# Kernel tuning notes

Hardware: AMD Instinct MI355X
Metric: run time of the kernel (lower is better)

Reference implementation:

```python
import jax, jax.numpy as jnp
import numpy as np

N_NODES = 100000
N_EDGES = 1600000
IN_C = 128
HID = 128
LAT = 64
N_LAYERS = 3
N_GRAPHS = 1000


def setup_inputs() -> dict:
    key = jax.random.key(0)
    ks = jax.random.split(key, 16)
    x = jax.random.normal(ks[0], (N_NODES, IN_C), dtype=jnp.float32)
    edge_index = jax.random.randint(ks[1], (2, N_EDGES), 0, N_NODES, dtype=jnp.int64)
    batch = jnp.sort(jax.random.randint(ks[2], (N_NODES,), 0, N_GRAPHS, dtype=jnp.int64))
    s = 1.0 / np.sqrt(HID)
    # per-layer GIN MLP params (in_c == hidden for all layers since IN_C == HID)
    W1 = jax.random.normal(ks[3], (N_LAYERS, IN_C, HID), dtype=jnp.float32) * s
    b1 = jnp.zeros((N_LAYERS, HID), dtype=jnp.float32)
    W2 = jax.random.normal(ks[4], (N_LAYERS, HID, HID), dtype=jnp.float32) * s
    b2 = jnp.zeros((N_LAYERS, HID), dtype=jnp.float32)
    W_mu = jax.random.normal(ks[5], (HID, LAT), dtype=jnp.float32) * s
    b_mu = jnp.zeros((LAT,), dtype=jnp.float32)
    W_lv = jax.random.normal(ks[6], (HID, LAT), dtype=jnp.float32) * s
    b_lv = jnp.zeros((LAT,), dtype=jnp.float32)
    return {"x": x, "edge_index": edge_index, "batch": batch,
            "W1": W1, "b1": b1, "W2": W2, "b2": b2,
            "W_mu": W_mu, "b_mu": b_mu, "W_lv": W_lv, "b_lv": b_lv}


def reference(x, edge_index, batch, W1, b1, W2, b2, W_mu, b_mu, W_lv, b_lv):
    src, dst = edge_index[0], edge_index[1]
    h = x
    for i in range(N_LAYERS):
        # GINConv (eps=0): h' = MLP(h + sum_{j in N(i)} h_j); scatter-add over edges
        agg = h + jax.ops.segment_sum(h[src], dst, num_segments=N_NODES)
        h = jax.nn.relu(agg @ W1[i] + b1[i])
        h = jax.nn.relu(h @ W2[i] + b2[i])
        h = jax.nn.relu(h)  # extra ReLU in forward after conv (idempotent here)
    # global_add_pool: segment-sum nodes into graphs
    g = jax.ops.segment_sum(h, batch, num_segments=N_GRAPHS)  # [G, HID]
    mu = g @ W_mu + b_mu
    logvar = g @ W_lv + b_lv
    return (mu, logvar)
```

## Files before the change

### kernel.cpp

```cpp
#include <hip/hip_runtime.h>

#define N_NODES 100000
#define N_EDGES 1600000
#define HID 128
#define LAT 64
#define N_LAYERS 3
#define N_GRAPHS 1000
#define CAP 64
#define NBIN 391
#define MAXBIN 4608
#define ACHUNK 8192
#define ABLOCKS ((N_EDGES + ACHUNK - 1) / ACHUNK)
#define CVT_BLOCKS (N_NODES * HID / 4 / 256)

typedef short bf16x8 __attribute__((ext_vector_type(8)));
typedef float f32x4 __attribute__((ext_vector_type(4)));

__device__ __forceinline__ float bf2f(unsigned short h) {
    union { unsigned int u; float f; } c;
    c.u = ((unsigned int)h) << 16;
    return c.f;
}
__device__ __forceinline__ unsigned short f2bf(float f) {
    union { float f; unsigned int u; } c;
    c.f = f;
    unsigned int u = c.u;
    return (unsigned short)((u + 0x7fffu + ((u >> 16) & 1u)) >> 16);
}
__device__ __forceinline__ unsigned int pack2(float a, float b) {
    return (unsigned int)f2bf(a) | ((unsigned int)f2bf(b) << 16);
}
__device__ __forceinline__ void addrow(float* acc, uint4 w) {
    acc[0] += bf2f((unsigned short)w.x); acc[1] += bf2f((unsigned short)(w.x >> 16));
    acc[2] += bf2f((unsigned short)w.y); acc[3] += bf2f((unsigned short)(w.y >> 16));
    acc[4] += bf2f((unsigned short)w.z); acc[5] += bf2f((unsigned short)(w.z >> 16));
    acc[6] += bf2f((unsigned short)w.w); acc[7] += bf2f((unsigned short)(w.w >> 16));
}

__global__ __launch_bounds__(256) void prep_kernel(const float* __restrict__ x,
                                                   unsigned short* __restrict__ xb,
                                                   const float* __restrict__ W1,
                                                   const float* __restrict__ W2,
                                                   unsigned short* __restrict__ Wt) {
    int blk = blockIdx.x;
    if (blk < 6) {
        const float* W = ((blk & 1) ? W2 : W1) + (size_t)(blk >> 1) * HID * HID;
        unsigned short* D = Wt + (size_t)blk * HID * HID;
        for (int idx = threadIdx.x; idx < HID * HID; idx += 256) {
            int n = idx >> 7, k = idx & 127;
            D[n * HID + k] = f2bf(W[k * HID + n]);
        }
        return;
    }
    int i = (blk - 6) * 256 + threadIdx.x;
    if (i >= N_NODES * HID / 4) return;
    float4 v = ((const float4*)x)[i];
    ((uint2*)xb)[i] = make_uint2(pack2(v.x, v.y), pack2(v.z, v.w));
}

__global__ __launch_bounds__(256) void binA_kernel(const int* __restrict__ ei,
                                                   int* __restrict__ gcnt,
                                                   unsigned int* __restrict__ ebin) {
    __shared__ unsigned int scount[NBIN];
    __shared__ unsigned int sfill[NBIN];
    int t = threadIdx.x;
    int base = blockIdx.x * ACHUNK;
    int n = N_EDGES - base;
    if (n > ACHUNK) n = ACHUNK;
    for (int i = t; i < NBIN; i += 256) scount[i] = 0u;
    __syncthreads();
    for (int i = t; i < n; i += 256) {
        int d = ei[N_EDGES + base + i];
        atomicAdd(&scount[d >> 8], 1u);
    }
    __syncthreads();
    for (int b = t; b < NBIN; b += 256) {
        unsigned int c = scount[b];
        sfill[b] = c ? (unsigned int)atomicAdd(&gcnt[b], (int)c) : 0u;
    }
    __syncthreads();
    for (int i = t; i < n; i += 256) {
        int s = ei[base + i];
        int d = ei[N_EDGES + base + i];
        int b = d >> 8;
        unsigned int pos = atomicAdd(&sfill[b], 1u);
        ebin[(size_t)b * MAXBIN + pos] = ((unsigned int)(d & 255) << 24) | (unsigned int)s;
    }
}

__global__ __launch_bounds__(256) void binB_kernel(const unsigned int* __restrict__ ebin,
                                                   const int* __restrict__ gcnt,
                                                   int* __restrict__ cnt,
                                                   int* __restrict__ csr) {
    __shared__ int scnt[256];
    int b = blockIdx.x;
    int t = threadIdx.x;
    scnt[t] = 0;
    __syncthreads();
    int n0 = b << 8;
    int c = gcnt[b];
    const unsigned int* src = ebin + (size_t)b * MAXBIN;
    for (int i = t; i < c; i += 256) {
        unsigned int e = src[i];
        int dl = (int)(e >> 24);
        int slot = atomicAdd(&scnt[dl], 1);
        csr[(size_t)(n0 + dl) * CAP + slot] = (int)(e & 0xFFFFFFu);
    }
    __syncthreads();
    int node = n0 + t;
    if (node < N_NODES) cnt[node] = scnt[t];
}

__global__ __launch_bounds__(256) void gather_kernel(const unsigned short* __restrict__ h,
                                                     const int* __restrict__ cnt,
                                                     const int* __restrict__ csr,
                                                     unsigned short* __restrict__ agg) {
    int t = threadIdx.x;
    int node = blockIdx.x * 16 + (t >> 4);
    int q = t & 15;
    if (node >= N_NODES) return;
    const int* nl = csr + (size_t)node * CAP;
    int deg = cnt[node];
    float acc[8] = {0.f, 0.f, 0.f, 0.f, 0.f, 0.f, 0.f, 0.f};
    addrow(acc, *(const uint4*)(h + (size_t)node * HID + q * 8));
    int e = 0;
    for (; e + 8 <= deg; e += 8) {
        int s0 = nl[e], s1 = nl[e + 1], s2 = nl[e + 2], s3 = nl[e + 3];
        int s4 = nl[e + 4], s5 = nl[e + 5], s6 = nl[e + 6], s7 = nl[e + 7];
        uint4 w0 = *(const uint4*)(h + (size_t)s0 * HID + q * 8);
        uint4 w1 = *(const uint4*)(h + (size_t)s1 * HID + q * 8);
        uint4 w2 = *(const uint4*)(h + (size_t)s2 * HID + q * 8);
        uint4 w3 = *(const uint4*)(h + (size_t)s3 * HID + q * 8);
        uint4 w4 = *(const uint4*)(h + (size_t)s4 * HID + q * 8);
        uint4 w5 = *(const uint4*)(h + (size_t)s5 * HID + q * 8);
        uint4 w6 = *(const uint4*)(h + (size_t)s6 * HID + q * 8);
        uint4 w7 = *(const uint4*)(h + (size_t)s7 * HID + q * 8);
        addrow(acc, w0); addrow(acc, w1); addrow(acc, w2); addrow(acc, w3);
        addrow(acc, w4); addrow(acc, w5); addrow(acc, w6); addrow(acc, w7);
    }
    for (; e + 4 <= deg; e += 4) {
        int s0 = nl[e], s1 = nl[e + 1], s2 = nl[e + 2], s3 = nl[e + 3];
        uint4 w0 = *(const uint4*)(h + (size_t)s0 * HID + q * 8);
        uint4 w1 = *(const uint4*)(h + (size_t)s1 * HID + q * 8);
        uint4 w2 = *(const uint4*)(h + (size_t)s2 * HID + q * 8);
        uint4 w3 = *(const uint4*)(h + (size_t)s3 * HID + q * 8);
        addrow(acc, w0); addrow(acc, w1); addrow(acc, w2); addrow(acc, w3);
    }
    for (; e < deg; ++e) {
        addrow(acc, *(const uint4*)(h + (size_t)nl[e] * HID + q * 8));
    }
    uint4 o;
    o.x = pack2(acc[0], acc[1]);
    o.y = pack2(acc[2], acc[3]);
    o.z = pack2(acc[4], acc[5]);
    o.w = pack2(acc[6], acc[7]);
    *(uint4*)(agg + (size_t)node * HID + q * 8) = o;
}

__global__ __launch_bounds__(256) void mlp_kernel(const unsigned short* __restrict__ A,
                                                  const unsigned short* __restrict__ W1t,
                                                  const float* __restrict__ b1,
                                                  const unsigned short* __restrict__ W2t,
                                                  const float* __restrict__ b2,
                                                  unsigned short* __restrict__ out,
                                                  const int* __restrict__ batch,
                                                  float* __restrict__ gpool) {
    __shared__ unsigned short sA[64][136];
    __shared__ unsigned short sW[128][40];
    __shared__ float sb[128];
    __shared__ int sbatch[64];
    const int t = threadIdx.x;
    const int w = t >> 6;
    const int l = t & 63;
    const int lm = l & 15;
    const int quad = l >> 4;
    const int row0 = blockIdx.x * 64;

    for (int idx = t; idx < 1024; idx += 256) {
        int r = idx >> 4, c = idx & 15;
        int grow = row0 + r;
        uint4 v = make_uint4(0u, 0u, 0u, 0u);
        if (grow < N_NODES) v = *(const uint4*)(A + (size_t)grow * HID + c * 8);
        *(uint4*)&sA[r][c * 8] = v;
    }
    if (gpool && t < 64) {
        int n = row0 + t;
        sbatch[t] = (n < N_NODES) ? batch[n] : -1;
    }

    const unsigned short* Wt[2] = {W1t, W2t};
    const float* bias[2] = {b1, b2};

    for (int p = 0; p < 2; ++p) {
        if (t < 128) sb[t] = bias[p][t];
        f32x4 acc[8];
#pragma unroll
        for (int nt = 0; nt < 8; ++nt) acc[nt] = (f32x4){0.f, 0.f, 0.f, 0.f};

        for (int kc = 0; kc < 4; ++kc) {
            __syncthreads();
            for (int idx = t; idx < 512; idx += 256) {
                int n = idx >> 2, kq = idx & 3;
                *(uint4*)&sW[n][kq * 8] =
                    *(const uint4*)(Wt[p] + (size_t)n * HID + kc * 32 + kq * 8);
            }
            __syncthreads();
            bf16x8 a = *(const bf16x8*)&sA[w * 16 + lm][kc * 32 + quad * 8];
#pragma unroll
            for (int nt = 0; nt < 8; ++nt) {
                bf16x8 b = *(const bf16x8*)&sW[nt * 16 + lm][quad * 8];
                acc[nt] = __builtin_amdgcn_mfma_f32_16x16x32_bf16(a, b, acc[nt], 0, 0, 0);
            }
        }
        __syncthreads();
#pragma unroll
        for (int nt = 0; nt < 8; ++nt) {
            float bv = sb[nt * 16 + lm];
#pragma unroll
            for (int r = 0; r < 4; ++r) {
                int m = w * 16 + quad * 4 + r;
                float val = fmaxf(acc[nt][r] + bv, 0.f);
                sA[m][nt * 16 + lm] = f2bf(val);
            }
        }
        __syncthreads();
    }

    if (!gpool) {
        for (int idx = t; idx < 1024; idx += 256) {
            int r = idx >> 4, c = idx & 15;
            int grow = row0 + r;
            if (grow < N_NODES)
                *(uint4*)(out + (size_t)grow * HID + c * 8) = *(const uint4*)&sA[r][c * 8];
        }
    } else {
        int c = t & 127;
        int r0 = (t >> 7) * 32;
        float acc = 0.f;
        int cur = sbatch[r0];
        for (int r = r0; r < r0 + 32; ++r) {
            int b = sbatch[r];
            if (b < 0) break;
            if (b != cur) {
                atomicAdd(&gpool[(size_t)cur * HID + c], acc);
                acc = 0.f;
                cur = b;
            }
            acc += bf2f(sA[r][c]);
        }
        if (cur >= 0) atomicAdd(&gpool[(size_t)cur * HID + c], acc);
    }
}

__global__ __launch_bounds__(128) void head_kernel(const float* __restrict__ g,
                                                   const float* __restrict__ Wmu,
                                                   const float* __restrict__ bmu,
                                                   const float* __restrict__ Wlv,
                                                   const float* __restrict__ blv,
                                                   float* __restrict__ out) {
    __shared__ float sg[HID];
    int gi = blockIdx.x;
    sg[threadIdx.x] = g[(size_t)gi * HID + threadIdx.x];
    __syncthreads();
    int j = threadIdx.x & 63;
    bool is_lv = threadIdx.x >= 64;
    const float* W = is_lv ? Wlv : Wmu;
    float acc = is_lv ? blv[j] : bmu[j];
    for (int k = 0; k < HID; ++k) acc = fmaf(sg[k], W[k * LAT + j], acc);
    out[(is_lv ? (size_t)N_GRAPHS * LAT : 0) + (size_t)gi * LAT + j] = acc;
}

extern "C" void kernel_launch(void* const* d_in, const int* in_sizes, int n_in,
                              void* d_out, int out_size, void* d_ws, size_t ws_size,
                              hipStream_t stream) {
    const float* x     = (const float*)d_in[0];
    const int*   ei    = (const int*)d_in[1];
    const int*   batch = (const int*)d_in[2];
    const float* W1    = (const float*)d_in[3];
    const float* b1    = (const float*)d_in[4];
    const float* W2    = (const float*)d_in[5];
    const float* b2    = (const float*)d_in[6];
    const float* Wmu   = (const float*)d_in[7];
    const float* bmu   = (const float*)d_in[8];
    const float* Wlv   = (const float*)d_in[9];
    const float* blv   = (const float*)d_in[10];
    float* out = (float*)d_out;

    unsigned short* xb   = (unsigned short*)d_ws;
    unsigned short* agg  = xb + (size_t)N_NODES * HID;
    unsigned short* hbuf = agg + (size_t)N_NODES * HID;
    int* csr = (int*)(hbuf + (size_t)N_NODES * HID);
    unsigned int* ebin = (unsigned int*)(csr + (size_t)N_NODES * CAP);
    unsigned short* Wt = (unsigned short*)(ebin + (size_t)NBIN * MAXBIN);
    float* g  = (float*)(Wt + (size_t)6 * HID * HID);
    int* gcnt = (int*)(g + (size_t)N_GRAPHS * HID);
    int* cnt  = gcnt + NBIN + 1;

    hipMemsetAsync(g, 0, (size_t)N_GRAPHS * HID * sizeof(float) + (NBIN + 1) * sizeof(int),
                   stream);

    binA_kernel<<<ABLOCKS, 256, 0, stream>>>(ei, gcnt, ebin);
    binB_kernel<<<NBIN, 256, 0, stream>>>(ebin, gcnt, cnt, csr);

    prep_kernel<<<CVT_BLOCKS + 6, 256, 0, stream>>>(x, xb, W1, W2, Wt);

    const unsigned short* hcur = xb;
    for (int i = 0; i < N_LAYERS; ++i) {
        bool last = (i == N_LAYERS - 1);
        gather_kernel<<<(N_NODES + 15) / 16, 256, 0, stream>>>(hcur, cnt, csr, agg);
        mlp_kernel<<<(N_NODES + 63) / 64, 256, 0, stream>>>(
            agg, Wt + (size_t)(2 * i) * HID * HID, b1 + (size_t)i * HID,
            Wt + (size_t)(2 * i + 1) * HID * HID, b2 + (size_t)i * HID, hbuf,
            batch, last ? g : nullptr);
        hcur = hbuf;
    }
    head_kernel<<<N_GRAPHS, 128, 0, stream>>>(g, Wmu, bmu, Wlv, blv, out);
}
```

Baseline: 419.3 us.

## Fuse neighbor gather into MLP kernel and ping-pong hidden buffers

Merges the per-layer gather and MLP kernels into one. Each 64-row block aggregates its nodes' neighbor rows straight into shared memory before the two matmuls. This removes the round trip of the agg buffer through global memory and one launch per layer. Two alternating h buffers replace the single one, since a fused layer cannot overwrite the h it is still reading. The cost is lower gather parallelism per block (4 sequential row groups per thread) and gather latency that is no longer overlapped across separate kernel waves.

```diff
diff --git a/kernel.cpp b/kernel.cpp
--- a/kernel.cpp
+++ b/kernel.cpp
@@ -111,60 +111,16 @@
     if (node < N_NODES) cnt[node] = scnt[t];
 }
 
-__global__ __launch_bounds__(256) void gather_kernel(const unsigned short* __restrict__ h,
-                                                     const int* __restrict__ cnt,
-                                                     const int* __restrict__ csr,
-                                                     unsigned short* __restrict__ agg) {
-    int t = threadIdx.x;
-    int node = blockIdx.x * 16 + (t >> 4);
-    int q = t & 15;
-    if (node >= N_NODES) return;
-    const int* nl = csr + (size_t)node * CAP;
-    int deg = cnt[node];
-    float acc[8] = {0.f, 0.f, 0.f, 0.f, 0.f, 0.f, 0.f, 0.f};
-    addrow(acc, *(const uint4*)(h + (size_t)node * HID + q * 8));
-    int e = 0;
-    for (; e + 8 <= deg; e += 8) {
-        int s0 = nl[e], s1 = nl[e + 1], s2 = nl[e + 2], s3 = nl[e + 3];
-        int s4 = nl[e + 4], s5 = nl[e + 5], s6 = nl[e + 6], s7 = nl[e + 7];
-        uint4 w0 = *(const uint4*)(h + (size_t)s0 * HID + q * 8);
-        uint4 w1 = *(const uint4*)(h + (size_t)s1 * HID + q * 8);
-        uint4 w2 = *(const uint4*)(h + (size_t)s2 * HID + q * 8);
-        uint4 w3 = *(const uint4*)(h + (size_t)s3 * HID + q * 8);
-        uint4 w4 = *(const uint4*)(h + (size_t)s4 * HID + q * 8);
-        uint4 w5 = *(const uint4*)(h + (size_t)s5 * HID + q * 8);
-        uint4 w6 = *(const uint4*)(h + (size_t)s6 * HID + q * 8);
-        uint4 w7 = *(const uint4*)(h + (size_t)s7 * HID + q * 8);
-        addrow(acc, w0); addrow(acc, w1); addrow(acc, w2); addrow(acc, w3);
-        addrow(acc, w4); addrow(acc, w5); addrow(acc, w6); addrow(acc, w7);
-    }
-    for (; e + 4 <= deg; e += 4) {
-        int s0 = nl[e], s1 = nl[e + 1], s2 = nl[e + 2], s3 = nl[e + 3];
-        uint4 w0 = *(const uint4*)(h + (size_t)s0 * HID + q * 8);
-        uint4 w1 = *(const uint4*)(h + (size_t)s1 * HID + q * 8);
-        uint4 w2 = *(const uint4*)(h + (size_t)s2 * HID + q * 8);
-        uint4 w3 = *(const uint4*)(h + (size_t)s3 * HID + q * 8);
-        addrow(acc, w0); addrow(acc, w1); addrow(acc, w2); addrow(acc, w3);
-    }
-    for (; e < deg; ++e) {
-        addrow(acc, *(const uint4*)(h + (size_t)nl[e] * HID + q * 8));
-    }
-    uint4 o;
-    o.x = pack2(acc[0], acc[1]);
-    o.y = pack2(acc[2], acc[3]);
-    o.z = pack2(acc[4], acc[5]);
-    o.w = pack2(acc[6], acc[7]);
-    *(uint4*)(agg + (size_t)node * HID + q * 8) = o;
-}
-
-__global__ __launch_bounds__(256) void mlp_kernel(const unsigned short* __restrict__ A,
-                                                  const unsigned short* __restrict__ W1t,
-                                                  const float* __restrict__ b1,
-                                                  const unsigned short* __restrict__ W2t,
-                                                  const float* __restrict__ b2,
-                                                  unsigned short* __restrict__ out,
-                                                  const int* __restrict__ batch,
-                                                  float* __restrict__ gpool) {
+__global__ __launch_bounds__(256) void fused_kernel(const unsigned short* __restrict__ h,
+                                                    const int* __restrict__ cnt,
+                                                    const int* __restrict__ csr,
+                                                    const unsigned short* __restrict__ W1t,
+                                                    const float* __restrict__ b1,
+                                                    const unsigned short* __restrict__ W2t,
+                                                    const float* __restrict__ b2,
+                                                    unsigned short* __restrict__ out,
+                                                    const int* __restrict__ batch,
+                                                    float* __restrict__ gpool) {
     __shared__ unsigned short sA[64][136];
     __shared__ unsigned short sW[128][40];
     __shared__ float sb[128];
@@ -176,16 +132,56 @@
     const int quad = l >> 4;
     const int row0 = blockIdx.x * 64;
 
-    for (int idx = t; idx < 1024; idx += 256) {
-        int r = idx >> 4, c = idx & 15;
-        int grow = row0 + r;
-        uint4 v = make_uint4(0u, 0u, 0u, 0u);
-        if (grow < N_NODES) v = *(const uint4*)(A + (size_t)grow * HID + c * 8);
-        *(uint4*)&sA[r][c * 8] = v;
-    }
     if (gpool && t < 64) {
         int n = row0 + t;
         sbatch[t] = (n < N_NODES) ? batch[n] : -1;
+    }
+
+    {
+        const int q = t & 15;
+        const int g16 = t >> 4;
+        for (int r4 = 0; r4 < 4; ++r4) {
+            int rloc = (r4 << 4) + g16;
+            int node = row0 + rloc;
+            float acc[8] = {0.f, 0.f, 0.f, 0.f, 0.f, 0.f, 0.f, 0.f};
+            if (node < N_NODES) {
+                addrow(acc, *(const uint4*)(h + (size_t)node * HID + q * 8));
+                const int* nl = csr + (size_t)node * CAP;
+                int deg = cnt[node];
+                int e = 0;
+                for (; e + 8 <= deg; e += 8) {
+                    int s0 = nl[e], s1 = nl[e + 1], s2 = nl[e + 2], s3 = nl[e + 3];
+                    int s4 = nl[e + 4], s5 = nl[e + 5], s6 = nl[e + 6], s7 = nl[e + 7];
+                    uint4 w0 = *(const uint4*)(h + (size_t)s0 * HID + q * 8);
+                    uint4 w1 = *(const uint4*)(h + (size_t)s1 * HID + q * 8);
+                    uint4 w2 = *(const uint4*)(h + (size_t)s2 * HID + q * 8);
+                    uint4 w3 = *(const uint4*)(h + (size_t)s3 * HID + q * 8);
+                    uint4 w4 = *(const uint4*)(h + (size_t)s4 * HID + q * 8);
+                    uint4 w5 = *(const uint4*)(h + (size_t)s5 * HID + q * 8);
+                    uint4 w6 = *(const uint4*)(h + (size_t)s6 * HID + q * 8);
+                    uint4 w7 = *(const uint4*)(h + (size_t)s7 * HID + q * 8);
+                    addrow(acc, w0); addrow(acc, w1); addrow(acc, w2); addrow(acc, w3);
+                    addrow(acc, w4); addrow(acc, w5); addrow(acc, w6); addrow(acc, w7);
+                }
+                for (; e + 4 <= deg; e += 4) {
+                    int s0 = nl[e], s1 = nl[e + 1], s2 = nl[e + 2], s3 = nl[e + 3];
+                    uint4 w0 = *(const uint4*)(h + (size_t)s0 * HID + q * 8);
+                    uint4 w1 = *(const uint4*)(h + (size_t)s1 * HID + q * 8);
+                    uint4 w2 = *(const uint4*)(h + (size_t)s2 * HID + q * 8);
+                    uint4 w3 = *(const uint4*)(h + (size_t)s3 * HID + q * 8);
+                    addrow(acc, w0); addrow(acc, w1); addrow(acc, w2); addrow(acc, w3);
+                }
+                for (; e < deg; ++e) {
+                    addrow(acc, *(const uint4*)(h + (size_t)nl[e] * HID + q * 8));
+                }
+            }
+            uint4 o;
+            o.x = pack2(acc[0], acc[1]);
+            o.y = pack2(acc[2], acc[3]);
+            o.z = pack2(acc[4], acc[5]);
+            o.w = pack2(acc[6], acc[7]);
+            *(uint4*)&sA[rloc][q * 8] = o;
+        }
     }
 
     const unsigned short* Wt[2] = {W1t, W2t};
@@ -287,9 +283,9 @@
     float* out = (float*)d_out;
 
     unsigned short* xb   = (unsigned short*)d_ws;
-    unsigned short* agg  = xb + (size_t)N_NODES * HID;
-    unsigned short* hbuf = agg + (size_t)N_NODES * HID;
-    int* csr = (int*)(hbuf + (size_t)N_NODES * HID);
+    unsigned short* h1   = xb + (size_t)N_NODES * HID;
+    unsigned short* h2   = h1 + (size_t)N_NODES * HID;
+    int* csr = (int*)(h2 + (size_t)N_NODES * HID);
     unsigned int* ebin = (unsigned int*)(csr + (size_t)N_NODES * CAP);
     unsigned short* Wt = (unsigned short*)(ebin + (size_t)NBIN * MAXBIN);
     float* g  = (float*)(Wt + (size_t)6 * HID * HID);
@@ -305,14 +301,16 @@
     prep_kernel<<<CVT_BLOCKS + 6, 256, 0, stream>>>(x, xb, W1, W2, Wt);
 
     const unsigned short* hcur = xb;
+    unsigned short* hdst = h1;
     for (int i = 0; i < N_LAYERS; ++i) {
         bool last = (i == N_LAYERS - 1);
-        gather_kernel<<<(N_NODES + 15) / 16, 256, 0, stream>>>(hcur, cnt, csr, agg);
-        mlp_kernel<<<(N_NODES + 63) / 64, 256, 0, stream>>>(
-            agg, Wt + (size_t)(2 * i) * HID * HID, b1 + (size_t)i * HID,
-            Wt + (size_t)(2 * i + 1) * HID * HID, b2 + (size_t)i * HID, hbuf,
-            batch, last ? g : nullptr);
-        hcur = hbuf;
+        fused_kernel<<<(N_NODES + 63) / 64, 256, 0, stream>>>(
+            hcur, cnt, csr,
+            Wt + (size_t)(2 * i) * HID * HID, b1 + (size_t)i * HID,
+            Wt + (size_t)(2 * i + 1) * HID * HID, b2 + (size_t)i * HID,
+            hdst, batch, last ? g : nullptr);
+        hcur = hdst;
+        hdst = (hdst == h1) ? h2 : h1;
     }
     head_kernel<<<N_GRAPHS, 128, 0, stream>>>(g, Wmu, bmu, Wlv, blv, out);
 }
```

Result: slower. 454.5 us (+8.4%).

## Merge setup kernels, stage CSR in LDS, prefetch MLP weights into registers

Applied to the files above, without the earlier changes.

The edge-binning pass is merged with the x/weight bf16 conversion into a single launch, removing one kernel launch and letting the two independent jobs run concurrently. binB now runs two blocks per bin, each building a 128-node half of the CSR in shared memory and then writing it out with coalesced int4 stores instead of scattered global writes. The MLP kernel register-prefetches the next weight k-chunk while the current one is used, hiding global load latency between the LDS barriers. The cost is that every edge bin is read twice, binB needs 32KB of LDS per block, and the copy-out also writes the unused CSR slots.

```diff
diff --git a/kernel.cpp b/kernel.cpp
--- a/kernel.cpp
+++ b/kernel.cpp
@@ -37,34 +37,36 @@
     acc[6] += bf2f((unsigned short)w.w); acc[7] += bf2f((unsigned short)(w.w >> 16));
 }
 
-__global__ __launch_bounds__(256) void prep_kernel(const float* __restrict__ x,
-                                                   unsigned short* __restrict__ xb,
-                                                   const float* __restrict__ W1,
-                                                   const float* __restrict__ W2,
-                                                   unsigned short* __restrict__ Wt) {
-    int blk = blockIdx.x;
-    if (blk < 6) {
-        const float* W = ((blk & 1) ? W2 : W1) + (size_t)(blk >> 1) * HID * HID;
-        unsigned short* D = Wt + (size_t)blk * HID * HID;
-        for (int idx = threadIdx.x; idx < HID * HID; idx += 256) {
-            int n = idx >> 7, k = idx & 127;
-            D[n * HID + k] = f2bf(W[k * HID + n]);
-        }
-        return;
-    }
-    int i = (blk - 6) * 256 + threadIdx.x;
-    if (i >= N_NODES * HID / 4) return;
-    float4 v = ((const float4*)x)[i];
-    ((uint2*)xb)[i] = make_uint2(pack2(v.x, v.y), pack2(v.z, v.w));
-}
-
-__global__ __launch_bounds__(256) void binA_kernel(const int* __restrict__ ei,
-                                                   int* __restrict__ gcnt,
-                                                   unsigned int* __restrict__ ebin) {
+__global__ __launch_bounds__(256) void setup_kernel(const int* __restrict__ ei,
+                                                    int* __restrict__ gcnt,
+                                                    unsigned int* __restrict__ ebin,
+                                                    const float* __restrict__ x,
+                                                    unsigned short* __restrict__ xb,
+                                                    const float* __restrict__ W1,
+                                                    const float* __restrict__ W2,
+                                                    unsigned short* __restrict__ Wt) {
     __shared__ unsigned int scount[NBIN];
     __shared__ unsigned int sfill[NBIN];
     int t = threadIdx.x;
-    int base = blockIdx.x * ACHUNK;
+    int blk = blockIdx.x;
+    if (blk >= ABLOCKS) {
+        int b2 = blk - ABLOCKS;
+        if (b2 < 6) {
+            const float* W = ((b2 & 1) ? W2 : W1) + (size_t)(b2 >> 1) * HID * HID;
+            unsigned short* D = Wt + (size_t)b2 * HID * HID;
+            for (int idx = t; idx < HID * HID; idx += 256) {
+                int n = idx >> 7, k = idx & 127;
+                D[n * HID + k] = f2bf(W[k * HID + n]);
+            }
+            return;
+        }
+        int i = (b2 - 6) * 256 + t;
+        if (i >= N_NODES * HID / 4) return;
+        float4 v = ((const float4*)x)[i];
+        ((uint2*)xb)[i] = make_uint2(pack2(v.x, v.y), pack2(v.z, v.w));
+        return;
+    }
+    int base = blk * ACHUNK;
     int n = N_EDGES - base;
     if (n > ACHUNK) n = ACHUNK;
     for (int i = t; i < NBIN; i += 256) scount[i] = 0u;
@@ -92,23 +94,33 @@
                                                    const int* __restrict__ gcnt,
                                                    int* __restrict__ cnt,
                                                    int* __restrict__ csr) {
-    __shared__ int scnt[256];
-    int b = blockIdx.x;
+    __shared__ int lcsr[128][CAP];
+    __shared__ int scnt[128];
+    int blk = blockIdx.x;
+    int b = blk >> 1;
+    int half = blk & 1;
     int t = threadIdx.x;
-    scnt[t] = 0;
-    __syncthreads();
-    int n0 = b << 8;
+    if (t < 128) scnt[t] = 0;
+    __syncthreads();
     int c = gcnt[b];
     const unsigned int* src = ebin + (size_t)b * MAXBIN;
     for (int i = t; i < c; i += 256) {
         unsigned int e = src[i];
         int dl = (int)(e >> 24);
-        int slot = atomicAdd(&scnt[dl], 1);
-        csr[(size_t)(n0 + dl) * CAP + slot] = (int)(e & 0xFFFFFFu);
-    }
-    __syncthreads();
-    int node = n0 + t;
-    if (node < N_NODES) cnt[node] = scnt[t];
+        if ((dl >> 7) == half) {
+            int slot = atomicAdd(&scnt[dl & 127], 1);
+            lcsr[dl & 127][slot] = (int)(e & 0xFFFFFFu);
+        }
+    }
+    __syncthreads();
+    int n0 = (b << 8) + (half << 7);
+    if (t < 128 && n0 + t < N_NODES) cnt[n0 + t] = scnt[t];
+    int nv = N_NODES - n0;
+    if (nv > 128) nv = 128;
+    if (nv < 0) nv = 0;
+    int4* dst = (int4*)(csr + (size_t)n0 * CAP);
+    const int4* ls = (const int4*)&lcsr[0][0];
+    for (int i = t; i < nv * (CAP / 4); i += 256) dst[i] = ls[i];
 }
 
 __global__ __launch_bounds__(256) void gather_kernel(const unsigned short* __restrict__ h,
@@ -188,8 +200,14 @@
         sbatch[t] = (n < N_NODES) ? batch[n] : -1;
     }
 
-    const unsigned short* Wt[2] = {W1t, W2t};
+    const unsigned short* Wt2[2] = {W1t, W2t};
     const float* bias[2] = {b1, b2};
+
+    const int n_0 = t >> 2;
+    const int n_1 = (t >> 2) + 64;
+    const int kq = t & 3;
+    uint4 rw0 = *(const uint4*)(W1t + (size_t)n_0 * HID + kq * 8);
+    uint4 rw1 = *(const uint4*)(W1t + (size_t)n_1 * HID + kq * 8);
 
     for (int p = 0; p < 2; ++p) {
         if (t < 128) sb[t] = bias[p][t];
@@ -199,12 +217,16 @@
 
         for (int kc = 0; kc < 4; ++kc) {
             __syncthreads();
-            for (int idx = t; idx < 512; idx += 256) {
-                int n = idx >> 2, kq = idx & 3;
-                *(uint4*)&sW[n][kq * 8] =
-                    *(const uint4*)(Wt[p] + (size_t)n * HID + kc * 32 + kq * 8);
-            }
+            *(uint4*)&sW[n_0][kq * 8] = rw0;
+            *(uint4*)&sW[n_1][kq * 8] = rw1;
             __syncthreads();
+            int s = (p << 2) + kc;
+            if (s < 7) {
+                int pn = (s + 1) >> 2, kn = (s + 1) & 3;
+                const unsigned short* Wn = Wt2[pn];
+                rw0 = *(const uint4*)(Wn + (size_t)n_0 * HID + kn * 32 + kq * 8);
+                rw1 = *(const uint4*)(Wn + (size_t)n_1 * HID + kn * 32 + kq * 8);
+            }
             bf16x8 a = *(const bf16x8*)&sA[w * 16 + lm][kc * 32 + quad * 8];
 #pragma unroll
             for (int nt = 0; nt < 8; ++nt) {
@@ -299,10 +321,9 @@
     hipMemsetAsync(g, 0, (size_t)N_GRAPHS * HID * sizeof(float) + (NBIN + 1) * sizeof(int),
                    stream);
 
-    binA_kernel<<<ABLOCKS, 256, 0, stream>>>(ei, gcnt, ebin);
-    binB_kernel<<<NBIN, 256, 0, stream>>>(ebin, gcnt, cnt, csr);
-
-    prep_kernel<<<CVT_BLOCKS + 6, 256, 0, stream>>>(x, xb, W1, W2, Wt);
+    setup_kernel<<<ABLOCKS + 6 + CVT_BLOCKS, 256, 0, stream>>>(ei, gcnt, ebin,
+                                                               x, xb, W1, W2, Wt);
+    binB_kernel<<<NBIN * 2, 256, 0, stream>>>(ebin, gcnt, cnt, csr);
 
     const unsigned short* hcur = xb;
     for (int i = 0; i < N_LAYERS; ++i) {
```

After: 408.6 us. -2.6%, faster.
